# Kernel optimization log

Measured on AMD Instinct MI355X. Metric: run time of the kernel, lower is better.

## Reference

```python
import jax, jax.numpy as jnp
import numpy as np


def _lstm_layer(x, w_ih, w_hh, b_ih, b_hh):
    """Single LSTM layer, batch_first x: [B, T, D] -> [B, T, H]. Gate order i,f,g,o."""
    B, T, _ = x.shape
    H = w_hh.shape[1]
    # Precompute input-to-gates for all timesteps: [B, T, 4H]
    xg = jnp.einsum('btd,gd->btg', x, w_ih) + b_ih + b_hh

    def step(carry, xg_t):
        h, c = carry
        g = xg_t + h @ w_hh.T  # [B, 4H]
        i, f, gg, o = jnp.split(g, 4, axis=-1)
        i = jax.nn.sigmoid(i)
        f = jax.nn.sigmoid(f)
        gg = jnp.tanh(gg)
        o = jax.nn.sigmoid(o)
        c = f * c + i * gg
        h = o * jnp.tanh(c)
        return (h, c), h

    h0 = jnp.zeros((B, H), x.dtype)
    (_, _), hs = jax.lax.scan(step, (h0, h0), jnp.swapaxes(xg, 0, 1))
    return jnp.swapaxes(hs, 0, 1)  # [B, T, H]


def setup_inputs() -> dict:
    key = jax.random.key(0)
    ks = jax.random.split(key, 11)
    B, T, E, H = 128, 512, 256, 512
    s_e = 1.0 / np.sqrt(H)
    inp = {
        'x': jax.random.normal(ks[0], (B, T, E), jnp.float32),
        'w_ih0': jax.random.uniform(ks[1], (4 * H, E), jnp.float32, -s_e, s_e),
        'w_hh0': jax.random.uniform(ks[2], (4 * H, H), jnp.float32, -s_e, s_e),
        'b_ih0': jax.random.uniform(ks[3], (4 * H,), jnp.float32, -s_e, s_e),
        'b_hh0': jax.random.uniform(ks[4], (4 * H,), jnp.float32, -s_e, s_e),
        'w_ih1': jax.random.uniform(ks[5], (4 * H, H), jnp.float32, -s_e, s_e),
        'w_hh1': jax.random.uniform(ks[6], (4 * H, H), jnp.float32, -s_e, s_e),
        'b_ih1': jax.random.uniform(ks[7], (4 * H,), jnp.float32, -s_e, s_e),
        'b_hh1': jax.random.uniform(ks[8], (4 * H,), jnp.float32, -s_e, s_e),
        'w_fc': jax.random.uniform(ks[9], (1, H), jnp.float32, -s_e, s_e),
        'b_fc': jax.random.uniform(ks[10], (1,), jnp.float32, -s_e, s_e),
    }
    return inp


def reference(x, w_ih0, w_hh0, b_ih0, b_hh0, w_ih1, w_hh1, b_ih1, b_hh1, w_fc, b_fc):
    h1 = _lstm_layer(x, w_ih0, w_hh0, b_ih0, b_hh0)   # [B, T, H]
    h2 = _lstm_layer(h1, w_ih1, w_hh1, b_ih1, b_hh1)  # [B, T, H]
    last = h2[:, -1, :]                               # [B, H]
    out = last @ w_fc.T + b_fc                        # [B, 1]
    return jax.nn.sigmoid(out)
```

## Files before the change

### kernel.cpp

```cpp
#include <hip/hip_runtime.h>

using u16    = unsigned short;
using u64_t  = unsigned long long;
using short4v = __attribute__((ext_vector_type(4))) short;
using short8 = __attribute__((ext_vector_type(8))) short;
using f32x4  = __attribute__((ext_vector_type(4))) float;

#define T_STEPS 512
#define BATCH   128
#define HDIM    512
#define EDIM    256
#define NWG     256
#define WGS     256
#define HPITCH  65536

__device__ __forceinline__ u16 f2bf(float f) {
  unsigned u = __float_as_uint(f);
  u += 0x7FFFu + ((u >> 16) & 1u);
  return (u16)(u >> 16);
}
__device__ __forceinline__ float bf2f(u16 h) {
  return __uint_as_float(((unsigned)h) << 16);
}
__device__ __forceinline__ float sigm(float x) { return 1.0f / (1.0f + __expf(-x)); }
__device__ __forceinline__ float ftanh(float x) { return 1.0f - 2.0f / (__expf(2.0f * x) + 1.0f); }

__device__ __forceinline__ u64_t cl8(const u16* p) {
  return __hip_atomic_load((const u64_t*)p, __ATOMIC_RELAXED, __HIP_MEMORY_SCOPE_AGENT);
}
__device__ __forceinline__ void cstore2(u16* p, u16 v) {
  __hip_atomic_store(p, v, __ATOMIC_RELAXED, __HIP_MEMORY_SCOPE_AGENT);
}
__device__ __forceinline__ short8 mk8(u64_t lo, u64_t hi) {
  short4v a = __builtin_bit_cast(short4v, lo);
  short4v b = __builtin_bit_cast(short4v, hi);
  return __builtin_shufflevector(a, b, 0, 1, 2, 3, 4, 5, 6, 7);
}

__global__ void cvt_bf16_kernel(const float* __restrict__ src, u16* __restrict__ dst, int n4) {
  int i = blockIdx.x * blockDim.x + threadIdx.x;
  if (i >= n4) return;
  float4 v = ((const float4*)src)[i];
  uint2 o;
  o.x = (unsigned)f2bf(v.x) | ((unsigned)f2bf(v.y) << 16);
  o.y = (unsigned)f2bf(v.z) | ((unsigned)f2bf(v.w) << 16);
  ((uint2*)dst)[i] = o;
}

__device__ __forceinline__ void grid_barrier(int* cnt, int* root, int* rel,
                                             int it, int tid, int bid) {
  __syncthreads();
  if (tid == 0) {
    int* mycnt = cnt + (bid >> 5) * 64;
    int old = __hip_atomic_fetch_add(mycnt, 1, __ATOMIC_RELAXED, __HIP_MEMORY_SCOPE_AGENT);
    if (old == 32 * (it + 1) - 1) {
      int r = __hip_atomic_fetch_add(root, 1, __ATOMIC_RELAXED, __HIP_MEMORY_SCOPE_AGENT);
      if (r == 8 * (it + 1) - 1)
        __hip_atomic_store(rel, it + 1, __ATOMIC_RELAXED, __HIP_MEMORY_SCOPE_AGENT);
    }
    while (__hip_atomic_load(rel, __ATOMIC_RELAXED, __HIP_MEMORY_SCOPE_AGENT) < it + 1)
      __builtin_amdgcn_s_sleep(1);
  }
  __syncthreads();
}

__global__ void __launch_bounds__(WGS, 1) lstm_kernel(
    const float* __restrict__ wih0, const float* __restrict__ whh0,
    const float* __restrict__ bih0, const float* __restrict__ bhh0,
    const float* __restrict__ wih1, const float* __restrict__ whh1,
    const float* __restrict__ bih1, const float* __restrict__ bhh1,
    const float* __restrict__ wfc,  const float* __restrict__ bfc,
    const u16* __restrict__ xbf, u16* __restrict__ h0buf, u16* __restrict__ h1buf,
    float* __restrict__ out, int* cnt, int* root, int* rel, int hist)
{
  extern __shared__ u16 smem[];
  u16* Ws_in  = smem;
  u16* Ws_rec = smem + 16384;

  const int tid    = threadIdx.x;
  const int bid    = blockIdx.x;
  const int layer  = bid >> 7;
  const int lb     = bid & 127;
  const int mhalf  = lb & 1;
  const int nc     = lb >> 1;
  const int jbase  = nc * 8;
  const int w      = tid >> 6;
  const int lane   = tid & 63;
  const int l15    = lane & 15;
  const int q      = lane >> 4;
  const int wmbase = mhalf * 64 + w * 16;

  const int K_in = layer ? HDIM : EDIM;
  const float* Wih = layer ? wih1 : wih0;
  const float* Whh = layer ? whh1 : whh0;
  const float* Bih = layer ? bih1 : bih0;
  const float* Bhh = layer ? bhh1 : bhh0;

  for (int p = tid; p < 32 * (K_in / 8); p += WGS) {
    int c = p >> 5, n = p & 31;
    int grow = (n >> 3) * HDIM + jbase + (n & 7);
    const float* s = Wih + (size_t)grow * K_in + c * 8;
    u16* d = Ws_in + p * 8;
    #pragma unroll
    for (int e = 0; e < 8; ++e) d[e] = f2bf(s[e]);
  }
  for (int p = tid; p < 32 * (HDIM / 8); p += WGS) {
    int c = p >> 5, n = p & 31;
    int grow = (n >> 3) * HDIM + jbase + (n & 7);
    const float* s = Whh + (size_t)grow * HDIM + c * 8;
    u16* d = Ws_rec + p * 8;
    #pragma unroll
    for (int e = 0; e < 8; ++e) d[e] = f2bf(s[e]);
  }

  const int cc = l15 & 7;
  const float bi_i = Bih[0*HDIM + jbase + cc] + Bhh[0*HDIM + jbase + cc];
  const float bi_f = Bih[1*HDIM + jbase + cc] + Bhh[1*HDIM + jbase + cc];
  const float bi_g = Bih[2*HDIM + jbase + cc] + Bhh[2*HDIM + jbase + cc];
  const float bi_o = Bih[3*HDIM + jbase + cc] + Bhh[3*HDIM + jbase + cc];

  __syncthreads();

  float cst[4] = {0.f, 0.f, 0.f, 0.f};
  u16* ownbuf = layer ? h1buf : h0buf;
  const int arow = wmbase + l15;
  const size_t cbase = ((size_t)q * 128 + arow) * 8;

  for (int it = 0; it <= T_STEPS; ++it) {
    const int t = layer ? (it - 1) : it;
    if (t >= 0 && t < T_STEPS) {
      short8 ifr[16];
      short8 rfr[16];
      short8 xfr[8];

      if (layer == 1) {
        const u16* ab = h0buf + (size_t)(hist ? t : (t & 1)) * HPITCH + cbase;
        if (hist) {
          #pragma unroll
          for (int kk = 0; kk < 16; ++kk)
            ifr[kk] = *(const short8*)(ab + kk * 4096);
        } else {
          #pragma unroll
          for (int kk = 0; kk < 16; ++kk)
            ifr[kk] = mk8(cl8(ab + kk * 4096), cl8(ab + kk * 4096 + 4));
        }
      }
      if (t > 0) {
        const u16* rb = ownbuf + (size_t)(hist ? (t - 1) : ((t - 1) & 1)) * HPITCH + cbase;
        if (hist) {
          #pragma unroll
          for (int kk = 0; kk < 16; ++kk)
            rfr[kk] = *(const short8*)(rb + kk * 4096);
        } else {
          #pragma unroll
          for (int kk = 0; kk < 16; ++kk)
            rfr[kk] = mk8(cl8(rb + kk * 4096), cl8(rb + kk * 4096 + 4));
        }
      }
      if (layer == 0) {
        const u16* xb = xbf + ((size_t)arow * T_STEPS + t) * EDIM + q * 8;
        #pragma unroll
        for (int kk = 0; kk < 8; ++kk) xfr[kk] = *(const short8*)(xb + kk * 32);
      }

      f32x4 acc0 = {0.f, 0.f, 0.f, 0.f};
      f32x4 acc1 = {0.f, 0.f, 0.f, 0.f};
      auto MM2 = [&](short8 a, const u16* Ws, int kk) {
        const u16* bb = Ws + (kk * 4 + q) * 256 + l15 * 8;
        short8 b0 = *(const short8*)bb;
        short8 b1 = *(const short8*)(bb + 128);
        acc0 = __builtin_amdgcn_mfma_f32_16x16x32_bf16(a, b0, acc0, 0, 0, 0);
        acc1 = __builtin_amdgcn_mfma_f32_16x16x32_bf16(a, b1, acc1, 0, 0, 0);
      };

      if (layer == 0) {
        #pragma unroll
        for (int kk = 0; kk < 8; ++kk) MM2(xfr[kk], Ws_in, kk);
      } else {
        #pragma unroll
        for (int kk = 0; kk < 16; ++kk) MM2(ifr[kk], Ws_in, kk);
      }
      if (t > 0) {
        #pragma unroll
        for (int kk = 0; kk < 16; ++kk) MM2(rfr[kk], Ws_rec, kk);
      }

      u16* hw = ownbuf + (size_t)(hist ? t : (t & 1)) * HPITCH + (size_t)nc * 1024;
      const bool low = (l15 < 8);
      #pragma unroll
      for (int r = 0; r < 4; ++r) {
        float a0 = acc0[r], a1 = acc1[r];
        float p0 = __shfl_xor(a0, 8);
        float p1 = __shfl_xor(a1, 8);
        float iv = low ? a0 : p0;
        float fv = low ? p0 : a0;
        float gv = low ? a1 : p1;
        float ov = low ? p1 : a1;
        iv = sigm(iv + bi_i);
        fv = sigm(fv + bi_f);
        gv = ftanh(gv + bi_g);
        ov = sigm(ov + bi_o);
        float cn = fv * cst[r] + iv * gv;
        cst[r] = cn;
        float hv = ov * ftanh(cn);
        if (low) cstore2(&hw[(size_t)(wmbase + q * 4 + r) * 8 + cc], f2bf(hv));
      }
    }
    grid_barrier(cnt, root, rel, it, tid, bid);
  }

  if (bid == NWG - 1) {
    __builtin_amdgcn_fence(__ATOMIC_ACQUIRE, "agent");
    const int b = tid >> 1, half = tid & 1;
    const u16* hp = h1buf + (size_t)(hist ? (T_STEPS - 1) : 1) * HPITCH;
    const float* wf = wfc + half * 256;
    float s = 0.f;
    for (int cg = 0; cg < 32; ++cg) {
      const u16* p = hp + ((size_t)(half * 32 + cg) * 128 + b) * 8;
      #pragma unroll
      for (int e = 0; e < 8; ++e) s += bf2f(p[e]) * wf[cg * 8 + e];
    }
    s += __shfl_xor(s, 1);
    if (half == 0) out[b] = sigm(s + bfc[0]);
  }
}

extern "C" void kernel_launch(void* const* d_in, const int* in_sizes, int n_in,
                              void* d_out, int out_size, void* d_ws, size_t ws_size,
                              hipStream_t stream) {
  (void)in_sizes; (void)n_in; (void)out_size;
  const float* x    = (const float*)d_in[0];
  const float* wih0 = (const float*)d_in[1];
  const float* whh0 = (const float*)d_in[2];
  const float* bih0 = (const float*)d_in[3];
  const float* bhh0 = (const float*)d_in[4];
  const float* wih1 = (const float*)d_in[5];
  const float* whh1 = (const float*)d_in[6];
  const float* bih1 = (const float*)d_in[7];
  const float* bhh1 = (const float*)d_in[8];
  const float* wfc  = (const float*)d_in[9];
  const float* bfc  = (const float*)d_in[10];
  float* outp = (float*)d_out;

  char* ws = (char*)d_ws;
  int*  cnt  = (int*)ws;
  int*  root = (int*)(ws + 2048);
  int*  rel  = (int*)(ws + 2176);
  u16*  xbf  = (u16*)(ws + 4096);
  u16*  h0   = (u16*)(ws + 4096 + 33554432);

  const size_t need_hist = 4096ull + 33554432ull + 2ull * T_STEPS * HPITCH * sizeof(u16);
  const int hist = (ws_size >= need_hist) ? 1 : 0;
  const size_t slots = hist ? T_STEPS : 2;
  u16* h1 = h0 + slots * HPITCH;

  hipMemsetAsync(d_ws, 0, 4096, stream);

  const int n4 = (BATCH * T_STEPS * EDIM) / 4;
  cvt_bf16_kernel<<<n4 / 256, 256, 0, stream>>>(x, xbf, n4);

  hipFuncSetAttribute((const void*)lstm_kernel,
                      hipFuncAttributeMaxDynamicSharedMemorySize, 65536);

  void* args[] = { (void*)&wih0, (void*)&whh0, (void*)&bih0, (void*)&bhh0,
                   (void*)&wih1, (void*)&whh1, (void*)&bih1, (void*)&bhh1,
                   (void*)&wfc,  (void*)&bfc,
                   (void*)&xbf,  (void*)&h0,   (void*)&h1,
                   (void*)&outp, (void*)&cnt,  (void*)&root, (void*)&rel,
                   (void*)&hist };
  hipLaunchCooperativeKernel((void*)lstm_kernel, dim3(NWG), dim3(WGS),
                             args, 65536, stream);
}
```

Measured before the change: 2.676 ms.

## Replace global grid barrier with per-group dataflow flags in history mode

In history mode, the single grid-wide barrier per step is replaced by four independent groups (layer × batch half). Each group keeps a hierarchical counter and per-subgroup release flags. Layer 0 waits only on its own group's previous step, and layer 1 waits on its own group and on the matching layer-0 group, so layer 0 can run ahead and the layers pipeline without a full-grid synchronisation. MFMA accumulation is also split into two interleaved accumulator chains to shorten the dependency chain, at the cost of an extra vector add and more sync state in the workspace.

```diff
diff --git a/kernel.cpp b/kernel.cpp
--- a/kernel.cpp
+++ b/kernel.cpp
@@ -30,6 +30,9 @@
 }
 __device__ __forceinline__ void cstore2(u16* p, u16 v) {
   __hip_atomic_store(p, v, __ATOMIC_RELAXED, __HIP_MEMORY_SCOPE_AGENT);
+}
+__device__ __forceinline__ int ld4(const int* p) {
+  return __hip_atomic_load(p, __ATOMIC_RELAXED, __HIP_MEMORY_SCOPE_AGENT);
 }
 __device__ __forceinline__ short8 mk8(u64_t lo, u64_t hi) {
   short4v a = __builtin_bit_cast(short4v, lo);
@@ -46,6 +49,7 @@
   o.y = (unsigned)f2bf(v.z) | ((unsigned)f2bf(v.w) << 16);
   ((uint2*)dst)[i] = o;
 }
+
 
 __device__ __forceinline__ void grid_barrier(int* cnt, int* root, int* rel,
                                              int it, int tid, int bid) {
@@ -71,7 +75,7 @@
     const float* __restrict__ bih1, const float* __restrict__ bhh1,
     const float* __restrict__ wfc,  const float* __restrict__ bfc,
     const u16* __restrict__ xbf, u16* __restrict__ h0buf, u16* __restrict__ h1buf,
-    float* __restrict__ out, int* cnt, int* root, int* rel, int hist)
+    float* __restrict__ out, int* syncp, int hist)
 {
   extern __shared__ u16 smem[];
   u16* Ws_in  = smem;
@@ -89,6 +93,9 @@
   const int l15    = lane & 15;
   const int q      = lane >> 4;
   const int wmbase = mhalf * 64 + w * 16;
+  const int gid    = layer * 2 + mhalf;
+
+  char* sb = (char*)syncp;
 
   const int K_in = layer ? HDIM : EDIM;
   const float* Wih = layer ? wih1 : wih0;
@@ -126,66 +133,69 @@
   const int arow = wmbase + l15;
   const size_t cbase = ((size_t)q * 128 + arow) * 8;
 
-  for (int it = 0; it <= T_STEPS; ++it) {
-    const int t = layer ? (it - 1) : it;
-    if (t >= 0 && t < T_STEPS) {
+  auto MM2 = [&](short8 a, const u16* Ws, int kk, f32x4& A0, f32x4& A1) {
+    const u16* bb = Ws + (kk * 4 + q) * 256 + l15 * 8;
+    short8 b0 = *(const short8*)bb;
+    short8 b1 = *(const short8*)(bb + 128);
+    A0 = __builtin_amdgcn_mfma_f32_16x16x32_bf16(a, b0, A0, 0, 0, 0);
+    A1 = __builtin_amdgcn_mfma_f32_16x16x32_bf16(a, b1, A1, 0, 0, 0);
+  };
+
+  if (hist) {
+    const int* own_rel = (const int*)(sb + 20480 + (size_t)(gid * 8 + (nc >> 3)) * 256);
+    const int* l0_rel  = (const int*)(sb + 20480 + (size_t)(mhalf * 8 + (nc >> 3)) * 256);
+    int* sub_cnt = (int*)(sb + (size_t)gid * 4096 + (size_t)(nc >> 3) * 256);
+    int* root_cnt = (int*)(sb + 16384 + (size_t)gid * 256);
+
+    for (int t = 0; t < T_STEPS; ++t) {
+      short8 xfr[8];
+      if (layer == 0) {
+        const u16* xb = xbf + ((size_t)arow * T_STEPS + t) * EDIM + q * 8;
+        #pragma unroll
+        for (int kk = 0; kk < 8; ++kk) xfr[kk] = *(const short8*)(xb + kk * 32);
+      }
+
+      if (tid == 0) {
+        if (layer == 0) {
+          if (t > 0) while (ld4(own_rel) < t) {}
+        } else {
+          while (ld4(own_rel) < t || ld4(l0_rel) < t + 1) {}
+        }
+      }
+      __syncthreads();
+
       short8 ifr[16];
       short8 rfr[16];
-      short8 xfr[8];
-
       if (layer == 1) {
-        const u16* ab = h0buf + (size_t)(hist ? t : (t & 1)) * HPITCH + cbase;
-        if (hist) {
-          #pragma unroll
-          for (int kk = 0; kk < 16; ++kk)
-            ifr[kk] = *(const short8*)(ab + kk * 4096);
-        } else {
-          #pragma unroll
-          for (int kk = 0; kk < 16; ++kk)
-            ifr[kk] = mk8(cl8(ab + kk * 4096), cl8(ab + kk * 4096 + 4));
-        }
+        const u16* ab = h0buf + (size_t)t * HPITCH + cbase;
+        #pragma unroll
+        for (int kk = 0; kk < 16; ++kk) ifr[kk] = *(const short8*)(ab + kk * 4096);
       }
       if (t > 0) {
-        const u16* rb = ownbuf + (size_t)(hist ? (t - 1) : ((t - 1) & 1)) * HPITCH + cbase;
-        if (hist) {
-          #pragma unroll
-          for (int kk = 0; kk < 16; ++kk)
-            rfr[kk] = *(const short8*)(rb + kk * 4096);
-        } else {
-          #pragma unroll
-          for (int kk = 0; kk < 16; ++kk)
-            rfr[kk] = mk8(cl8(rb + kk * 4096), cl8(rb + kk * 4096 + 4));
-        }
-      }
+        const u16* rb = ownbuf + (size_t)(t - 1) * HPITCH + cbase;
+        #pragma unroll
+        for (int kk = 0; kk < 16; ++kk) rfr[kk] = *(const short8*)(rb + kk * 4096);
+      }
+
+      f32x4 a0A = {0,0,0,0}, a1A = {0,0,0,0}, a0B = {0,0,0,0}, a1B = {0,0,0,0};
       if (layer == 0) {
-        const u16* xb = xbf + ((size_t)arow * T_STEPS + t) * EDIM + q * 8;
-        #pragma unroll
-        for (int kk = 0; kk < 8; ++kk) xfr[kk] = *(const short8*)(xb + kk * 32);
-      }
-
-      f32x4 acc0 = {0.f, 0.f, 0.f, 0.f};
-      f32x4 acc1 = {0.f, 0.f, 0.f, 0.f};
-      auto MM2 = [&](short8 a, const u16* Ws, int kk) {
-        const u16* bb = Ws + (kk * 4 + q) * 256 + l15 * 8;
-        short8 b0 = *(const short8*)bb;
-        short8 b1 = *(const short8*)(bb + 128);
-        acc0 = __builtin_amdgcn_mfma_f32_16x16x32_bf16(a, b0, acc0, 0, 0, 0);
-        acc1 = __builtin_amdgcn_mfma_f32_16x16x32_bf16(a, b1, acc1, 0, 0, 0);
-      };
-
-      if (layer == 0) {
-        #pragma unroll
-        for (int kk = 0; kk < 8; ++kk) MM2(xfr[kk], Ws_in, kk);
+        #pragma unroll
+        for (int kk = 0; kk < 8; ++kk)
+          MM2(xfr[kk], Ws_in, kk, (kk & 1) ? a0B : a0A, (kk & 1) ? a1B : a1A);
       } else {
         #pragma unroll
-        for (int kk = 0; kk < 16; ++kk) MM2(ifr[kk], Ws_in, kk);
+        for (int kk = 0; kk < 16; ++kk)
+          MM2(ifr[kk], Ws_in, kk, (kk & 1) ? a0B : a0A, (kk & 1) ? a1B : a1A);
       }
       if (t > 0) {
         #pragma unroll
-        for (int kk = 0; kk < 16; ++kk) MM2(rfr[kk], Ws_rec, kk);
-      }
-
-      u16* hw = ownbuf + (size_t)(hist ? t : (t & 1)) * HPITCH + (size_t)nc * 1024;
+        for (int kk = 0; kk < 16; ++kk)
+          MM2(rfr[kk], Ws_rec, kk, (kk & 1) ? a0B : a0A, (kk & 1) ? a1B : a1A);
+      }
+      f32x4 acc0 = a0A + a0B;
+      f32x4 acc1 = a1A + a1B;
+
+      u16* hw = ownbuf + (size_t)t * HPITCH + (size_t)nc * 1024;
       const bool low = (l15 < 8);
       #pragma unroll
       for (int r = 0; r < 4; ++r) {
@@ -205,14 +215,115 @@
         float hv = ov * ftanh(cn);
         if (low) cstore2(&hw[(size_t)(wmbase + q * 4 + r) * 8 + cc], f2bf(hv));
       }
-    }
-    grid_barrier(cnt, root, rel, it, tid, bid);
-  }
-
+
+      __syncthreads();
+      if (tid == 0) {
+        int old = __hip_atomic_fetch_add(sub_cnt, 1, __ATOMIC_RELAXED, __HIP_MEMORY_SCOPE_AGENT);
+        if (old == 8 * (t + 1) - 1) {
+          int r = __hip_atomic_fetch_add(root_cnt, 1, __ATOMIC_RELAXED, __HIP_MEMORY_SCOPE_AGENT);
+          if (r == 8 * (t + 1) - 1) {
+            #pragma unroll
+            for (int l = 0; l < 8; ++l)
+              __hip_atomic_store((int*)(sb + 20480 + (size_t)(gid * 8 + l) * 256), t + 1,
+                                 __ATOMIC_RELAXED, __HIP_MEMORY_SCOPE_AGENT);
+          }
+        }
+      }
+    }
+
+    if (bid == NWG - 1) {
+      const int* g2 = (const int*)(sb + 20480 + (size_t)(2 * 8 + 0) * 256);
+      const int* g3 = (const int*)(sb + 20480 + (size_t)(3 * 8 + 0) * 256);
+      if (tid == 0) { while (ld4(g2) < T_STEPS || ld4(g3) < T_STEPS) {} }
+      __syncthreads();
+      __builtin_amdgcn_fence(__ATOMIC_ACQUIRE, "agent");
+      const int b = tid >> 1, half = tid & 1;
+      const u16* hp = h1buf + (size_t)(T_STEPS - 1) * HPITCH;
+      const float* wf = wfc + half * 256;
+      float s = 0.f;
+      for (int cg = 0; cg < 32; ++cg) {
+        const u16* p = hp + ((size_t)(half * 32 + cg) * 128 + b) * 8;
+        #pragma unroll
+        for (int e = 0; e < 8; ++e) s += bf2f(p[e]) * wf[cg * 8 + e];
+      }
+      s += __shfl_xor(s, 1);
+      if (half == 0) out[b] = sigm(s + bfc[0]);
+    }
+    return;
+  }
+
+  int* f_cnt  = (int*)(sb + 28672);
+  int* f_root = (int*)(sb + 30720);
+  int* f_rel  = (int*)(sb + 30848);
+  for (int it = 0; it <= T_STEPS; ++it) {
+    const int t = layer ? (it - 1) : it;
+    if (t >= 0 && t < T_STEPS) {
+      short8 ifr[16];
+      short8 rfr[16];
+      short8 xfr[8];
+      if (layer == 1) {
+        const u16* ab = h0buf + (size_t)(t & 1) * HPITCH + cbase;
+        #pragma unroll
+        for (int kk = 0; kk < 16; ++kk)
+          ifr[kk] = mk8(cl8(ab + kk * 4096), cl8(ab + kk * 4096 + 4));
+      }
+      if (t > 0) {
+        const u16* rb = ownbuf + (size_t)((t - 1) & 1) * HPITCH + cbase;
+        #pragma unroll
+        for (int kk = 0; kk < 16; ++kk)
+          rfr[kk] = mk8(cl8(rb + kk * 4096), cl8(rb + kk * 4096 + 4));
+      }
+      if (layer == 0) {
+        const u16* xb = xbf + ((size_t)arow * T_STEPS + t) * EDIM + q * 8;
+        #pragma unroll
+        for (int kk = 0; kk < 8; ++kk) xfr[kk] = *(const short8*)(xb + kk * 32);
+      }
+
+      f32x4 a0A = {0,0,0,0}, a1A = {0,0,0,0}, a0B = {0,0,0,0}, a1B = {0,0,0,0};
+      if (layer == 0) {
+        #pragma unroll
+        for (int kk = 0; kk < 8; ++kk)
+          MM2(xfr[kk], Ws_in, kk, (kk & 1) ? a0B : a0A, (kk & 1) ? a1B : a1A);
+      } else {
+        #pragma unroll
+        for (int kk = 0; kk < 16; ++kk)
+          MM2(ifr[kk], Ws_in, kk, (kk & 1) ? a0B : a0A, (kk & 1) ? a1B : a1A);
+      }
+      if (t > 0) {
+        #pragma unroll
+        for (int kk = 0; kk < 16; ++kk)
+          MM2(rfr[kk], Ws_rec, kk, (kk & 1) ? a0B : a0A, (kk & 1) ? a1B : a1A);
+      }
+      f32x4 acc0 = a0A + a0B;
+      f32x4 acc1 = a1A + a1B;
+
+      u16* hw = ownbuf + (size_t)(t & 1) * HPITCH + (size_t)nc * 1024;
+      const bool low = (l15 < 8);
+      #pragma unroll
+      for (int r = 0; r < 4; ++r) {
+        float a0 = acc0[r], a1 = acc1[r];
+        float p0 = __shfl_xor(a0, 8);
+        float p1 = __shfl_xor(a1, 8);
+        float iv = low ? a0 : p0;
+        float fv = low ? p0 : a0;
+        float gv = low ? a1 : p1;
+        float ov = low ? p1 : a1;
+        iv = sigm(iv + bi_i);
+        fv = sigm(fv + bi_f);
+        gv = ftanh(gv + bi_g);
+        ov = sigm(ov + bi_o);
+        float cn = fv * cst[r] + iv * gv;
+        cst[r] = cn;
+        float hv = ov * ftanh(cn);
+        if (low) cstore2(&hw[(size_t)(wmbase + q * 4 + r) * 8 + cc], f2bf(hv));
+      }
+    }
+    grid_barrier(f_cnt, f_root, f_rel, it, tid, bid);
+  }
   if (bid == NWG - 1) {
     __builtin_amdgcn_fence(__ATOMIC_ACQUIRE, "agent");
     const int b = tid >> 1, half = tid & 1;
-    const u16* hp = h1buf + (size_t)(hist ? (T_STEPS - 1) : 1) * HPITCH;
+    const u16* hp = h1buf + (size_t)1 * HPITCH;
     const float* wf = wfc + half * 256;
     float s = 0.f;
     for (int cg = 0; cg < 32; ++cg) {
@@ -243,18 +354,16 @@
   float* outp = (float*)d_out;
 
   char* ws = (char*)d_ws;
-  int*  cnt  = (int*)ws;
-  int*  root = (int*)(ws + 2048);
-  int*  rel  = (int*)(ws + 2176);
-  u16*  xbf  = (u16*)(ws + 4096);
-  u16*  h0   = (u16*)(ws + 4096 + 33554432);
-
-  const size_t need_hist = 4096ull + 33554432ull + 2ull * T_STEPS * HPITCH * sizeof(u16);
+  int*  syncp = (int*)ws;
+  u16*  xbf   = (u16*)(ws + 32768);
+  u16*  h0    = (u16*)(ws + 32768 + 33554432);
+
+  const size_t need_hist = 32768ull + 33554432ull + 2ull * T_STEPS * HPITCH * sizeof(u16);
   const int hist = (ws_size >= need_hist) ? 1 : 0;
   const size_t slots = hist ? T_STEPS : 2;
   u16* h1 = h0 + slots * HPITCH;
 
-  hipMemsetAsync(d_ws, 0, 4096, stream);
+  hipMemsetAsync(d_ws, 0, 32768, stream);
 
   const int n4 = (BATCH * T_STEPS * EDIM) / 4;
   cvt_bf16_kernel<<<n4 / 256, 256, 0, stream>>>(x, xbf, n4);
@@ -266,8 +375,7 @@
                    (void*)&wih1, (void*)&whh1, (void*)&bih1, (void*)&bhh1,
                    (void*)&wfc,  (void*)&bfc,
                    (void*)&xbf,  (void*)&h0,   (void*)&h1,
-                   (void*)&outp, (void*)&cnt,  (void*)&root, (void*)&rel,
-                   (void*)&hist };
+                   (void*)&outp, (void*)&syncp, (void*)&hist };
   hipLaunchCooperativeKernel((void*)lstm_kernel, dim3(NWG), dim3(WGS),
                              args, 65536, stream);
 }
```

New measurement: 2.399 ms. 10.4% less time.
